# Optimization experiments

Hardware: AMD Instinct MI355X
Metric: run time of the kernel (lower is better)

Reference implementation:

```python
import jax, jax.numpy as jnp
import numpy as np
import math

PHI = (1 + math.sqrt(5)) / 2
ALPHA = 1 / PHI          # residual scale
BETA = 1 / PHI ** 2      # sparse-matmul scale
DIM = 1910
NZ = int(DIM * DIM / PHI)


def setup_inputs() -> dict:
    key = jax.random.key(0)
    kx, ki, kv = jax.random.split(key, 3)
    x = jax.random.normal(kx, (8, 4096, DIM), dtype=jnp.float32)
    W_indices = jax.random.randint(ki, (2, NZ), 0, DIM, dtype=jnp.int32)
    W_values = jax.random.normal(kv, (NZ,), dtype=jnp.float32) / math.sqrt(DIM)
    return {"x": x, "W_indices": W_indices, "W_values": W_values}


def reference(x, W_indices, W_values):
    dim = x.shape[-1]
    # COO -> dense: duplicate (row,col) entries sum, matching torch.sparse semantics.
    W = jnp.zeros((dim, dim), dtype=x.dtype).at[W_indices[0], W_indices[1]].add(W_values)
    orig_shape = x.shape
    xf = x.reshape(-1, dim)          # [tokens, dim]
    Wx = xf @ W.T                    # (W @ x.T).T == x @ W.T
    out = ALPHA * xf + BETA * Wx
    return out.reshape(orig_shape)
```

## Files before the change

### kernel.cpp

```cpp
#include <hip/hip_runtime.h>
#include <hip/hip_bf16.h>
#include <stdint.h>

#define DIMV 1910
#define KP   1920
#define NT   30
#define TT   120
#define PHI_F  1.6180339887498949f
#define BETA_F 0.3819660112501051f

typedef __attribute__((ext_vector_type(4))) float f32x4;
typedef __attribute__((ext_vector_type(8))) short bf16x8;
typedef __attribute__((ext_vector_type(8))) unsigned short u16x8;

__device__ __forceinline__ void gl16(const void* g, void* l) {
    __builtin_amdgcn_global_load_lds(
        (const __attribute__((address_space(1))) void*)(uintptr_t)g,
        (__attribute__((address_space(3))) void*)(uint32_t)(uintptr_t)l,
        16, 0, 0);
}

__global__ void k_prep(const float* __restrict__ x, unsigned short* __restrict__ xb, int total8,
                       const int* __restrict__ ridx, const int* __restrict__ cidx,
                       const float* __restrict__ vals, float* __restrict__ Wd, int nz) {
    const int tid  = threadIdx.x;
    const int half = (int)gridDim.x >> 1;
    const int b    = (int)blockIdx.x >> 1;
    const int stride = half * 256;
    if ((blockIdx.x & 1) == 0) {
        for (int i = b * 256 + tid; i < total8; i += stride) {
            int v = i * 8;
            int row = v / KP;
            int col = v - row * KP;
            u16x8 o;
            if (col + 8 <= DIMV) {
                const float2* s = (const float2*)(x + (size_t)row * DIMV + col);
                float2 f0 = s[0], f1 = s[1], f2 = s[2], f3 = s[3];
                float f[8] = {f0.x, f0.y, f1.x, f1.y, f2.x, f2.y, f3.x, f3.y};
#pragma unroll
                for (int j = 0; j < 8; ++j) {
                    __hip_bfloat16 bb = __float2bfloat16(f[j]);
                    o[j] = *reinterpret_cast<unsigned short*>(&bb);
                }
            } else {
#pragma unroll
                for (int j = 0; j < 8; ++j) {
                    int c = col + j;
                    float fv = (c < DIMV) ? x[(size_t)row * DIMV + c] : 0.f;
                    __hip_bfloat16 bb = __float2bfloat16(fv);
                    o[j] = *reinterpret_cast<unsigned short*>(&bb);
                }
            }
            *(u16x8*)(xb + (size_t)v) = o;
        }
    } else {
        for (int i = b * 256 + tid; i < nz; i += stride)
            atomicAdd(Wd + (size_t)ridx[i] * DIMV + cidx[i], vals[i]);
    }
}

__global__ void k_build_w(const float* __restrict__ Wd, unsigned short* __restrict__ Wb, int total8) {
    int stride = gridDim.x * blockDim.x;
    for (int i = blockIdx.x * blockDim.x + threadIdx.x; i < total8; i += stride) {
        int v = i * 8;
        int n = v / KP;
        int k = v - n * KP;
        u16x8 o;
#pragma unroll
        for (int j = 0; j < 8; ++j) {
            int kk = k + j;
            float fv = (n < DIMV && kk < DIMV) ? Wd[(size_t)n * DIMV + kk] : 0.f;
            if (kk == n && n < DIMV) fv += PHI_F;
            __hip_bfloat16 b = __float2bfloat16(fv);
            o[j] = *reinterpret_cast<unsigned short*>(&b);
        }
        *(u16x8*)(Wb + (size_t)v) = o;
    }
}

__global__ __launch_bounds__(512, 2) void k_gemm(const short* __restrict__ A,
                                                 const short* __restrict__ B,
                                                 float* __restrict__ C) {
    __shared__ char lds[131072];

    const int bid = blockIdx.x;
    const int bmg = bid & 31;
    const int bn  = bid >> 5;

    const int tid = threadIdx.x;
    const int w   = tid >> 6;
    const int l   = tid & 63;
    const int wm  = w >> 2;
    const int wn  = w & 3;
    const int fr  = l & 15;
    const int q   = l >> 4;

    const int    srow = tid >> 3;
    const size_t KPB  = (size_t)KP * 2;
    const int    swz  = ((tid & 7) ^ (srow & 7)) * 16;
    const char*  bSrc = (const char*)B + (size_t)(bn * 256 + srow) * KPB + swz;
    const size_t sweep = (size_t)64 * KPB;
    char* stDst = lds + tid * 16;

    const int co0  = ((q    ) ^ (fr & 7)) * 16;
    const int co1  = ((4 + q) ^ (fr & 7)) * 16;
    const int aOff = (wm * 128 + fr) * 128;
    const int bOff = (wn * 64 + fr) * 128;

    f32x4 acc[8][4] = {};
    bf16x8 aP0[8], aP1[8], bR0[4], bR1[4];

#define STAGE_A(src, kk_, slot, s) gl16((src) + (size_t)(s) * sweep + (size_t)(kk_) * 128, stDst + (slot) + (s) * 8192)
#define STAGE_B(kk_, slot, s)      gl16(bSrc  + (size_t)(s) * sweep + (size_t)(kk_) * 128, stDst + 65536 + (slot) + (s) * 8192)
#define MM(bank, bb)                                                             \
    _Pragma("unroll")                                                            \
    for (int mi = 0; mi < 8; ++mi)                                               \
        _Pragma("unroll")                                                        \
        for (int ni = 0; ni < 4; ++ni)                                           \
            acc[mi][ni] = __builtin_amdgcn_mfma_f32_16x16x32_bf16((bank)[mi], (bb)[ni], acc[mi][ni], 0, 0, 0);

    const char* aSrc0 = (const char*)A + (size_t)(bmg * 256 + srow) * KPB + swz;
    const size_t mstep = (size_t)8192 * KPB;

#pragma unroll
    for (int s = 0; s < 4; ++s) STAGE_A(aSrc0, 0, 0, s);
#pragma unroll
    for (int s = 0; s < 4; ++s) STAGE_B(0, 0, s);
#pragma unroll
    for (int s = 0; s < 4; ++s) STAGE_A(aSrc0, 1, 32768, s);
#pragma unroll
    for (int s = 0; s < 4; ++s) STAGE_B(1, 32768, s);
    asm volatile("s_waitcnt vmcnt(8)" ::: "memory");
    __builtin_amdgcn_s_barrier();
    __builtin_amdgcn_sched_barrier(0);
#pragma unroll
    for (int mi = 0; mi < 8; ++mi) aP0[mi] = *(const bf16x8*)(lds + aOff + mi * 2048 + co0);
#pragma unroll
    for (int ni = 0; ni < 4; ++ni) bR0[ni] = *(const bf16x8*)(lds + 65536 + bOff + ni * 2048 + co0);

    int bo  = 0;
    int k2  = 2;
    int tkR = 0, mtR = 0;
    const char* aStage = aSrc0;

    for (int t = 0; t < TT; ++t) {
        const int nbo = bo ^ 32768;
        const char* pa  = lds + bo + aOff;
        const char* pb  = lds + 65536 + bo + bOff;
        const char* paN = lds + nbo + aOff;
        const char* pbN = lds + 65536 + nbo + bOff;
        const bool haveN = (t + 1 < TT);
        const bool have2 = (t + 2 < TT);

        __builtin_amdgcn_s_barrier();
        __builtin_amdgcn_sched_barrier(0);
#pragma unroll
        for (int mi = 0; mi < 8; ++mi) aP1[mi] = *(const bf16x8*)(pa + mi * 2048 + co1);
#pragma unroll
        for (int ni = 0; ni < 4; ++ni) bR1[ni] = *(const bf16x8*)(pb + ni * 2048 + co1);
        __builtin_amdgcn_sched_barrier(0);
        __builtin_amdgcn_s_setprio(1);
        MM(aP0, bR0)
        __builtin_amdgcn_s_setprio(0);
        asm volatile("s_waitcnt vmcnt(0)" ::: "memory");
        asm volatile("s_waitcnt lgkmcnt(0)" ::: "memory");
        __builtin_amdgcn_sched_barrier(0);

        __builtin_amdgcn_s_barrier();
        __builtin_amdgcn_sched_barrier(0);
        if (haveN) {
#pragma unroll
            for (int mi = 0; mi < 8; ++mi) aP0[mi] = *(const bf16x8*)(paN + mi * 2048 + co0);
#pragma unroll
            for (int ni = 0; ni < 4; ++ni) bR0[ni] = *(const bf16x8*)(pbN + ni * 2048 + co0);
        }
        if (have2) {
            STAGE_A(aStage, k2, bo, 0); STAGE_A(aStage, k2, bo, 1);
            STAGE_A(aStage, k2, bo, 2); STAGE_A(aStage, k2, bo, 3);
            STAGE_B(k2, bo, 0); STAGE_B(k2, bo, 1);
            STAGE_B(k2, bo, 2); STAGE_B(k2, bo, 3);
        }
        __builtin_amdgcn_sched_barrier(0);
        __builtin_amdgcn_s_setprio(1);
        MM(aP1, bR1)
        __builtin_amdgcn_s_setprio(0);
        asm volatile("s_waitcnt vmcnt(8)" ::: "memory");
        asm volatile("s_waitcnt lgkmcnt(0)" ::: "memory");
        __builtin_amdgcn_sched_barrier(0);

        if (tkR == NT - 1) {
            const int bm    = mtR * 32 + bmg;
            const int grow0 = bm * 256 + wm * 128 + q * 4;
            const int gcol0 = bn * 256 + wn * 64 + fr;
#pragma unroll
            for (int ei = 0; ei < 8; ++ei) {
#pragma unroll
                for (int ni = 0; ni < 4; ++ni) {
                    int gcol = gcol0 + ni * 16;
                    if (gcol < DIMV) {
                        size_t base = (size_t)(grow0 + ei * 16) * DIMV + gcol;
#pragma unroll
                        for (int r = 0; r < 4; ++r)
                            C[base + (size_t)r * DIMV] = BETA_F * acc[ei][ni][r];
                    }
                }
            }
            if (haveN) {
#pragma unroll
                for (int ei = 0; ei < 8; ++ei)
#pragma unroll
                    for (int ni = 0; ni < 4; ++ni)
                        acc[ei][ni] = (f32x4)(0.f);
            }
            tkR = 0; ++mtR;
        } else ++tkR;

        bo = nbo;
        if (++k2 == NT) { k2 = 0; aStage += mstep; }
    }
#undef STAGE_A
#undef STAGE_B
#undef MM
}

extern "C" void kernel_launch(void* const* d_in, const int* in_sizes, int n_in,
                              void* d_out, int out_size, void* d_ws, size_t ws_size,
                              hipStream_t stream) {
    const float* x    = (const float*)d_in[0];
    const int*   widx = (const int*)d_in[1];
    const float* wval = (const float*)d_in[2];
    float* out = (float*)d_out;

    const int nz = in_sizes[2];
    const int M  = in_sizes[0] / DIMV;

    const size_t xb_bytes = (size_t)M * KP * 2;
    const size_t wb_bytes = (size_t)2048 * KP * 2;
    const size_t wd_bytes = (size_t)DIMV * DIMV * 4;
    char* ws = (char*)d_ws;
    unsigned short* xb = (unsigned short*)ws;
    unsigned short* Wb = (unsigned short*)(ws + xb_bytes);
    float*          Wd = (float*)(ws + xb_bytes + wb_bytes);
    if (ws_size < xb_bytes + wb_bytes + wd_bytes) return;

    hipMemsetAsync(Wd, 0, wd_bytes, stream);
    k_prep<<<2048, 256, 0, stream>>>(x, xb, M * KP / 8, widx, widx + nz, wval, Wd, nz);
    k_build_w<<<1800, 256, 0, stream>>>(Wd, Wb, KP * KP / 8);
    k_gemm<<<256, 512, 0, stream>>>((const short*)xb, (const short*)Wb, out);
}
```

Measured before the change: 404.4 us.

## Restructure GEMM to 256x128 tiles with 4-wave blocks and triple-buffered A

The persistent GEMM moves from 512-thread blocks with 256x256 output tiles and K-step 64 to 256-thread blocks with 256x128 tiles and K-step 32. It doubles the grid to 512 blocks and halves LDS per block. A is triple-buffered in LDS and B double-buffered, with separate staging points inside each K iteration. The aim is better occupancy and scheduling, at the cost of less reuse of A per tile, more barriers per unit of work, and B being loaded for twice as many column tiles.

New measurement: 458.6 us. 1.13x slower.

```diff
diff --git a/kernel.cpp b/kernel.cpp
--- a/kernel.cpp
+++ b/kernel.cpp
@@ -4,8 +4,8 @@
 
 #define DIMV 1910
 #define KP   1920
-#define NT   30
-#define TT   120
+#define NT   60
+#define TT   240
 #define PHI_F  1.6180339887498949f
 #define BETA_F 0.3819660112501051f
 
@@ -78,46 +78,40 @@
     }
 }
 
-__global__ __launch_bounds__(512, 2) void k_gemm(const short* __restrict__ A,
+__global__ __launch_bounds__(256, 2) void k_gemm(const short* __restrict__ A,
                                                  const short* __restrict__ B,
                                                  float* __restrict__ C) {
-    __shared__ char lds[131072];
+    __shared__ char lds[65536];
 
     const int bid = blockIdx.x;
-    const int bmg = bid & 31;
-    const int bn  = bid >> 5;
+    const int bn  = bid & 15;
+    const int bmg = bid >> 4;
 
     const int tid = threadIdx.x;
     const int w   = tid >> 6;
     const int l   = tid & 63;
-    const int wm  = w >> 2;
-    const int wn  = w & 3;
+    const int wm  = w >> 1;
+    const int wn  = w & 1;
     const int fr  = l & 15;
     const int q   = l >> 4;
 
-    const int    srow = tid >> 3;
+    const int    srow = tid >> 2;
+    const int    slt  = tid & 3;
     const size_t KPB  = (size_t)KP * 2;
-    const int    swz  = ((tid & 7) ^ (srow & 7)) * 16;
-    const char*  bSrc = (const char*)B + (size_t)(bn * 256 + srow) * KPB + swz;
+    const int    swz  = (slt ^ ((srow >> 1) & 3)) * 16;
+    const char*  bSrc = (const char*)B + (size_t)(bn * 128 + srow) * KPB + swz;
     const size_t sweep = (size_t)64 * KPB;
     char* stDst = lds + tid * 16;
 
-    const int co0  = ((q    ) ^ (fr & 7)) * 16;
-    const int co1  = ((4 + q) ^ (fr & 7)) * 16;
-    const int aOff = (wm * 128 + fr) * 128;
-    const int bOff = (wn * 64 + fr) * 128;
+    const int co   = (q ^ ((fr >> 1) & 3)) * 16;
+    const int aOff = (wm * 128 + fr) * 64 + co;
+    const int bOff = 49152 + (wn * 64 + fr) * 64 + co;
 
     f32x4 acc[8][4] = {};
-    bf16x8 aP0[8], aP1[8], bR0[4], bR1[4];
-
-#define STAGE_A(src, kk_, slot, s) gl16((src) + (size_t)(s) * sweep + (size_t)(kk_) * 128, stDst + (slot) + (s) * 8192)
-#define STAGE_B(kk_, slot, s)      gl16(bSrc  + (size_t)(s) * sweep + (size_t)(kk_) * 128, stDst + 65536 + (slot) + (s) * 8192)
-#define MM(bank, bb)                                                             \
-    _Pragma("unroll")                                                            \
-    for (int mi = 0; mi < 8; ++mi)                                               \
-        _Pragma("unroll")                                                        \
-        for (int ni = 0; ni < 4; ++ni)                                           \
-            acc[mi][ni] = __builtin_amdgcn_mfma_f32_16x16x32_bf16((bank)[mi], (bb)[ni], acc[mi][ni], 0, 0, 0);
+    bf16x8 aLo[4], aHi[4], b[4];
+
+#define STAGE_A(src, kk_, slot, s) gl16((src) + (size_t)(s) * sweep + (size_t)(kk_) * 64, stDst + (slot) + (s) * 4096)
+#define STAGE_B(kk_, slot, s)      gl16(bSrc  + (size_t)(s) * sweep + (size_t)(kk_) * 64, stDst + 49152 + (slot) + (s) * 4096)
 
     const char* aSrc0 = (const char*)A + (size_t)(bmg * 256 + srow) * KPB + swz;
     const size_t mstep = (size_t)8192 * KPB;
@@ -125,73 +119,69 @@
 #pragma unroll
     for (int s = 0; s < 4; ++s) STAGE_A(aSrc0, 0, 0, s);
 #pragma unroll
-    for (int s = 0; s < 4; ++s) STAGE_B(0, 0, s);
-#pragma unroll
-    for (int s = 0; s < 4; ++s) STAGE_A(aSrc0, 1, 32768, s);
-#pragma unroll
-    for (int s = 0; s < 4; ++s) STAGE_B(1, 32768, s);
-    asm volatile("s_waitcnt vmcnt(8)" ::: "memory");
+    for (int s = 0; s < 2; ++s) STAGE_B(0, 0, s);
+#pragma unroll
+    for (int s = 0; s < 4; ++s) STAGE_A(aSrc0, 1, 16384, s);
+    asm volatile("s_waitcnt vmcnt(4)" ::: "memory");
     __builtin_amdgcn_s_barrier();
-    __builtin_amdgcn_sched_barrier(0);
-#pragma unroll
-    for (int mi = 0; mi < 8; ++mi) aP0[mi] = *(const bf16x8*)(lds + aOff + mi * 2048 + co0);
-#pragma unroll
-    for (int ni = 0; ni < 4; ++ni) bR0[ni] = *(const bf16x8*)(lds + 65536 + bOff + ni * 2048 + co0);
-
-    int bo  = 0;
-    int k2  = 2;
+    asm volatile("" ::: "memory");
+
+    int boA = 0, stA = 32768;
+    int boB = 0;
+    int kb = 1, k2 = 2;
     int tkR = 0, mtR = 0;
     const char* aStage = aSrc0;
 
     for (int t = 0; t < TT; ++t) {
-        const int nbo = bo ^ 32768;
-        const char* pa  = lds + bo + aOff;
-        const char* pb  = lds + 65536 + bo + bOff;
-        const char* paN = lds + nbo + aOff;
-        const char* pbN = lds + 65536 + nbo + bOff;
-        const bool haveN = (t + 1 < TT);
-        const bool have2 = (t + 2 < TT);
-
-        __builtin_amdgcn_s_barrier();
-        __builtin_amdgcn_sched_barrier(0);
-#pragma unroll
-        for (int mi = 0; mi < 8; ++mi) aP1[mi] = *(const bf16x8*)(pa + mi * 2048 + co1);
-#pragma unroll
-        for (int ni = 0; ni < 4; ++ni) bR1[ni] = *(const bf16x8*)(pb + ni * 2048 + co1);
+        const char* pa = lds + boA + aOff;
+        const char* pb = lds + boB + bOff;
+        const bool stb = (t + 1 < TT);
+        const bool sta = (t + 2 < TT);
+
+#pragma unroll
+        for (int mi = 0; mi < 4; ++mi) aLo[mi] = *(const bf16x8*)(pa + mi * 1024);
+#pragma unroll
+        for (int ni = 0; ni < 4; ++ni) b[ni]   = *(const bf16x8*)(pb + ni * 1024);
+        if (stb) { STAGE_B(kb, boB ^ 8192, 0); STAGE_B(kb, boB ^ 8192, 1); }
+        asm volatile("" ::: "memory");
+        __builtin_amdgcn_s_barrier();
+        asm volatile("s_waitcnt lgkmcnt(0)" ::: "memory");
         __builtin_amdgcn_sched_barrier(0);
         __builtin_amdgcn_s_setprio(1);
-        MM(aP0, bR0)
+#pragma unroll
+        for (int mi = 0; mi < 4; ++mi)
+#pragma unroll
+            for (int ni = 0; ni < 4; ++ni)
+                acc[mi][ni] = __builtin_amdgcn_mfma_f32_16x16x32_bf16(aLo[mi], b[ni], acc[mi][ni], 0, 0, 0);
         __builtin_amdgcn_s_setprio(0);
-        asm volatile("s_waitcnt vmcnt(0)" ::: "memory");
+        asm volatile("" ::: "memory");
+        __builtin_amdgcn_s_barrier();
+        asm volatile("" ::: "memory");
+
+#pragma unroll
+        for (int mi = 0; mi < 4; ++mi) aHi[mi] = *(const bf16x8*)(pa + 4096 + mi * 1024);
+        if (sta) { STAGE_A(aStage, k2, stA, 0); STAGE_A(aStage, k2, stA, 1);
+                   STAGE_A(aStage, k2, stA, 2); STAGE_A(aStage, k2, stA, 3); }
+        asm volatile("" ::: "memory");
+        __builtin_amdgcn_s_barrier();
         asm volatile("s_waitcnt lgkmcnt(0)" ::: "memory");
         __builtin_amdgcn_sched_barrier(0);
-
-        __builtin_amdgcn_s_barrier();
-        __builtin_amdgcn_sched_barrier(0);
-        if (haveN) {
-#pragma unroll
-            for (int mi = 0; mi < 8; ++mi) aP0[mi] = *(const bf16x8*)(paN + mi * 2048 + co0);
-#pragma unroll
-            for (int ni = 0; ni < 4; ++ni) bR0[ni] = *(const bf16x8*)(pbN + ni * 2048 + co0);
-        }
-        if (have2) {
-            STAGE_A(aStage, k2, bo, 0); STAGE_A(aStage, k2, bo, 1);
-            STAGE_A(aStage, k2, bo, 2); STAGE_A(aStage, k2, bo, 3);
-            STAGE_B(k2, bo, 0); STAGE_B(k2, bo, 1);
-            STAGE_B(k2, bo, 2); STAGE_B(k2, bo, 3);
-        }
-        __builtin_amdgcn_sched_barrier(0);
         __builtin_amdgcn_s_setprio(1);
-        MM(aP1, bR1)
+#pragma unroll
+        for (int mi = 0; mi < 4; ++mi)
+#pragma unroll
+            for (int ni = 0; ni < 4; ++ni)
+                acc[mi + 4][ni] = __builtin_amdgcn_mfma_f32_16x16x32_bf16(aHi[mi], b[ni], acc[mi + 4][ni], 0, 0, 0);
         __builtin_amdgcn_s_setprio(0);
-        asm volatile("s_waitcnt vmcnt(8)" ::: "memory");
-        asm volatile("s_waitcnt lgkmcnt(0)" ::: "memory");
-        __builtin_amdgcn_sched_barrier(0);
+        if (sta) { asm volatile("s_waitcnt vmcnt(4)" ::: "memory"); }
+        else     { asm volatile("s_waitcnt vmcnt(0)" ::: "memory"); }
+        __builtin_amdgcn_s_barrier();
+        asm volatile("" ::: "memory");
 
         if (tkR == NT - 1) {
             const int bm    = mtR * 32 + bmg;
             const int grow0 = bm * 256 + wm * 128 + q * 4;
-            const int gcol0 = bn * 256 + wn * 64 + fr;
+            const int gcol0 = bn * 128 + wn * 64 + fr;
 #pragma unroll
             for (int ei = 0; ei < 8; ++ei) {
 #pragma unroll
@@ -205,7 +195,7 @@
                     }
                 }
             }
-            if (haveN) {
+            if (t + 1 < TT) {
 #pragma unroll
                 for (int ei = 0; ei < 8; ++ei)
 #pragma unroll
@@ -215,12 +205,14 @@
             tkR = 0; ++mtR;
         } else ++tkR;
 
-        bo = nbo;
+        boA = (boA == 32768) ? 0 : boA + 16384;
+        stA = (stA == 32768) ? 0 : stA + 16384;
+        boB ^= 8192;
+        if (++kb == NT) kb = 0;
         if (++k2 == NT) { k2 = 0; aStage += mstep; }
     }
 #undef STAGE_A
 #undef STAGE_B
-#undef MM
 }
 
 extern "C" void kernel_launch(void* const* d_in, const int* in_sizes, int n_in,
@@ -246,5 +238,5 @@
     hipMemsetAsync(Wd, 0, wd_bytes, stream);
     k_prep<<<2048, 256, 0, stream>>>(x, xb, M * KP / 8, widx, widx + nz, wval, Wd, nz);
     k_build_w<<<1800, 256, 0, stream>>>(Wd, Wb, KP * KP / 8);
-    k_gemm<<<256, 512, 0, stream>>>((const short*)xb, (const short*)Wb, out);
-}
+    k_gemm<<<512, 256, 0, stream>>>((const short*)xb, (const short*)Wb, out);
+}
```
